# Kernel tuning notes

Measured on AMD Instinct MI355X. Metric: run time of the kernel, lower is better.

Reference implementation:

```python
import jax, jax.numpy as jnp
import numpy as np


def setup_inputs() -> dict:
    key = jax.random.key(0)
    kD, kx, kc = jax.random.split(key, 3)
    B, N, I, O = 8, 20000, 64, 64
    KM = 8 * 32  # k_bands * m_samples = 256
    D = jax.random.normal(kD, (B, N, KM), dtype=jnp.float32)
    x = jax.random.normal(kx, (B, N, I), dtype=jnp.float32)
    coefficients = jax.random.normal(kc, (1, O, I, KM), dtype=jnp.float32)
    return {"D": D, "x": x, "coefficients": coefficients}


def reference(D, x, coefficients):
    # D: (B, N, M), x: (B, N, I), coefficients: (1, O, I, M)
    # Original: C = diag_embed(coeff) -> (1,O,I,M,M); einsum('boimj,bomi->boij')
    # Since C is diagonal in (m, j), that einsum is an elementwise scale:
    #   C_Dt_x[b,o,i,m] = coeff[o,i,m] * Dt_x[b,m,i]
    # and the final contraction + channel-sum is:
    #   out[b,n,o] = (1/sqrt(M)) * sum_m D[b,n,m] * sum_i coeff[o,i,m] * Dt_x[b,m,i]
    M = D.shape[2]
    coeff = coefficients[0]                              # (O, I, M)
    Dt_x = jnp.einsum('bnm,bni->bmi', D, x)              # (B, M, I)
    S = jnp.einsum('oim,bmi->bom', coeff, Dt_x)          # (B, O, M)
    out = jnp.einsum('bnm,bom->bno', D, S) / jnp.sqrt(jnp.asarray(M, D.dtype))
    return out  # (B, N, O)
```

## Files before the change

kernel.cpp:

```cpp
#include <hip/hip_runtime.h>

#define B 8
#define N 20000
#define M 256
#define I 64
#define O 64
#define MI (M * I)
#define KT 32
#define PW (MI / 2)
#define SSS 264
#define MSW(m) ((m) ^ (((m) >> 3) & 7))

typedef __attribute__((ext_vector_type(8))) short   bf16x8;
typedef __attribute__((ext_vector_type(4))) float   f32x4;
typedef __attribute__((ext_vector_type(4))) unsigned int uint4v;

__device__ __forceinline__ unsigned pk2bf(float lo, float hi) {
    unsigned r;
    asm("v_cvt_pk_bf16_f32 %0, %1, %2" : "=v"(r) : "v"(lo), "v"(hi));
    return r;
}

__device__ __forceinline__ unsigned short f2bf(float v) {
    unsigned a = __float_as_uint(v);
    return (unsigned short)((a + 0x7fffu + ((a >> 16) & 1u)) >> 16);
}

__device__ __forceinline__ void gload16(const float* src, float* lds) {
    __builtin_amdgcn_global_load_lds(
        (const __attribute__((address_space(1))) void*)src,
        (__attribute__((address_space(3))) void*)lds, 16, 0, 0);
}

__global__ __launch_bounds__(256) void stage1(const float* __restrict__ Dg,
                                              const float* __restrict__ xg,
                                              unsigned* __restrict__ partial,
                                              int chunk) {
    const int b = blockIdx.y, s = blockIdx.x;
    const int n0 = s * chunk;
    const int nend = min(n0 + chunk, N);
    const int tid = threadIdx.x;
    const int lane = tid & 63;
    const int w = tid >> 6;
    const int lg = lane >> 4;
    const int l15 = lane & 15;

    __shared__ float sD[4][2][KT * 64];
    __shared__ unsigned short sX[4][4 * 64 * 8];

    f32x4 acc[4][4];
#pragma unroll
    for (int a = 0; a < 4; ++a)
#pragma unroll
        for (int v = 0; v < 4; ++v) acc[a][v] = (f32x4){0.f, 0.f, 0.f, 0.f};

    const float* Db = Dg + (size_t)b * N * M;
    const float* xb = xg + (size_t)b * N * I;

    const int steps = (nend > n0) ? (nend - n0) >> 5 : 0;

    auto issueD = [&](int t) {
        const int nb = n0 + t * KT;
        float* slot = &sD[w][t & 1][0];
        const float* src = Db + (size_t)(nb + lg) * M + (w << 6) + (l15 << 2);
#pragma unroll
        for (int j = 0; j < 8; ++j)
            gload16(src + (size_t)(4 * j) * M, slot + j * 256);
    };

    float4 xreg[8];
    auto loadX = [&](int t) {
        const float* xp = &xb[(size_t)(n0 + t * KT + 8 * lg) * I + 4 * l15];
#pragma unroll
        for (int q = 0; q < 8; ++q)
            xreg[q] = *(const float4*)(xp + (size_t)q * I);
    };

    unsigned short* wX = sX[w];

    if (steps > 0) {
        issueD(0);
        if (steps > 1) issueD(1);
        loadX(0);

        for (int t = 0; t < steps; ++t) {
            const int p = t & 1;
#pragma unroll
            for (int j = 0; j < 4; ++j) {
                uint4v cx;
#pragma unroll
                for (int e = 0; e < 4; ++e)
                    cx[e] = pk2bf(((const float*)&xreg[2 * e])[j],
                                  ((const float*)&xreg[2 * e + 1])[j]);
                *(uint4v*)&wX[((size_t)lg * 64 + MSW(4 * l15 + j)) * 8] = cx;
            }
            bf16x8 bfr[4];
#pragma unroll
            for (int v = 0; v < 4; ++v)
                bfr[v] = *(const bf16x8*)&wX[((size_t)lg * 64 + MSW(v * 16 + l15)) * 8];
            if (t + 1 < steps) loadX(t + 1);
            const float* slot = &sD[w][p][0];
#pragma unroll
            for (int sm = 0; sm < 4; ++sm) {
                float fr[8];
#pragma unroll
                for (int r = 0; r < 8; ++r)
                    fr[r] = slot[(8 * lg + r) * 64 + sm * 16 + l15];
                uint4v pk = {pk2bf(fr[0], fr[1]), pk2bf(fr[2], fr[3]),
                             pk2bf(fr[4], fr[5]), pk2bf(fr[6], fr[7])};
                bf16x8 afr = __builtin_bit_cast(bf16x8, pk);
#pragma unroll
                for (int v = 0; v < 4; ++v)
                    acc[sm][v] = __builtin_amdgcn_mfma_f32_16x16x32_bf16(
                        afr, bfr[v], acc[sm][v], 0, 0, 0);
            }
            if (t + 2 < steps) issueD(t + 2);
        }
    }

    unsigned* pp = partial + ((size_t)s * B + b) * PW + (size_t)w * 2048 + lane;
#pragma unroll
    for (int sm = 0; sm < 4; ++sm)
#pragma unroll
        for (int v = 0; v < 4; ++v)
#pragma unroll
            for (int rp = 0; rp < 2; ++rp)
                pp[(sm * 8 + v * 2 + rp) * 64] =
                    pk2bf(acc[sm][v][2 * rp], acc[sm][v][2 * rp + 1]);
}

__global__ __launch_bounds__(256) void reduce_partials(const unsigned* __restrict__ partial,
                                                       float* __restrict__ dtx,
                                                       int nsplit) {
    const int bb = blockIdx.y;
    const int j = blockIdx.x * 256 + threadIdx.x;
    const int w    = j >> 11;
    const int rem  = j & 2047;
    const int c    = rem >> 6;
    const int lane = rem & 63;
    const int sm = c >> 3, v = (c >> 1) & 3, rp = c & 1;
    const int lg = lane >> 4, l15 = lane & 15;
    const int m0 = w * 64 + sm * 16 + lg * 4 + 2 * rp;
    const int i  = v * 16 + l15;

    const unsigned* p = partial + (size_t)bb * PW + j;
    float s0 = 0.f, s1 = 0.f;
#pragma unroll 4
    for (int s = 0; s < nsplit; ++s) {
        const unsigned word = p[(size_t)s * B * PW];
        s0 += __uint_as_float(word << 16);
        s1 += __uint_as_float(word & 0xFFFF0000u);
    }
    dtx[(size_t)bb * MI + (size_t)m0 * I + i]       = s0;
    dtx[(size_t)bb * MI + (size_t)(m0 + 1) * I + i] = s1;
}

__global__ __launch_bounds__(256) void stage2(const float* __restrict__ coeff,
                                              const float* __restrict__ dtx,
                                              unsigned short* __restrict__ ST) {
    const int g = blockIdx.x * 256 + threadIdx.x;
    const int b = g >> 14;
    const int rem = g & 16383;
    const int o = rem >> 8;
    const int m = rem & 255;
    const float* dt = dtx + (size_t)b * MI + (size_t)m * I;
    const float* cf = coeff + (size_t)o * I * M + m;
    float acc = 0.f;
#pragma unroll 8
    for (int i = 0; i < I; ++i)
        acc = fmaf(cf[(size_t)i * M], dt[i], acc);
    ST[((size_t)b * O + o) * M + m] = f2bf(acc * 0.0625f);
}

__global__ __launch_bounds__(256) void stage3(const float* __restrict__ Dg,
                                              const unsigned short* __restrict__ STg,
                                              float* __restrict__ outg) {
    const int b = blockIdx.y;
    const int n0 = blockIdx.x * 256;
    const int tid = threadIdx.x;
    const int lane = tid & 63;
    const int w = tid >> 6;

    __shared__ unsigned short sS[64 * SSS];

    {
        const int o = tid >> 2, seg = (tid & 3) * 64;
        const unsigned short* src = STg + ((size_t)b * O + o) * M + seg;
        unsigned short* dst = &sS[o * SSS + seg];
#pragma unroll
        for (int c = 0; c < 8; ++c)
            *(uint4v*)&dst[c * 8] = *(const uint4v*)&src[c * 8];
    }

    f32x4 acc[4][4];
#pragma unroll
    for (int a = 0; a < 4; ++a)
#pragma unroll
        for (int v = 0; v < 4; ++v) acc[a][v] = (f32x4){0.f, 0.f, 0.f, 0.f};

    __syncthreads();

    const float* Db = Dg + (size_t)b * N * M;
    const int k8 = (lane >> 4) << 3;

#pragma unroll 1
    for (int ks = 0; ks < 8; ++ks) {
        const int kb = ks * 32 + k8;
        bf16x8 bfr[4];
#pragma unroll
        for (int v = 0; v < 4; ++v)
            bfr[v] = *(const bf16x8*)&sS[(v * 16 + (lane & 15)) * SSS + kb];
#pragma unroll
        for (int sn = 0; sn < 4; ++sn) {
            int n = n0 + w * 64 + sn * 16 + (lane & 15);
            n = min(n, N - 1);
            const float* ap = Db + (size_t)n * M + kb;
            const float4 f0 = *(const float4*)ap;
            const float4 f1 = *(const float4*)(ap + 4);
            uint4v pk = {pk2bf(f0.x, f0.y), pk2bf(f0.z, f0.w),
                         pk2bf(f1.x, f1.y), pk2bf(f1.z, f1.w)};
            bf16x8 afr = __builtin_bit_cast(bf16x8, pk);
#pragma unroll
            for (int v = 0; v < 4; ++v)
                acc[sn][v] = __builtin_amdgcn_mfma_f32_16x16x32_bf16(
                    afr, bfr[v], acc[sn][v], 0, 0, 0);
        }
    }

#pragma unroll
    for (int sn = 0; sn < 4; ++sn)
#pragma unroll
        for (int v = 0; v < 4; ++v)
#pragma unroll
            for (int r = 0; r < 4; ++r) {
                const int n = n0 + w * 64 + sn * 16 + ((lane >> 4) << 2) + r;
                if (n < N)
                    outg[((size_t)b * N + n) * O + v * 16 + (lane & 15)] = acc[sn][v][r];
            }
}

extern "C" void kernel_launch(void* const* d_in, const int* in_sizes, int n_in,
                              void* d_out, int out_size, void* d_ws, size_t ws_size,
                              hipStream_t stream) {
    const float* Dg    = (const float*)d_in[0];
    const float* xg    = (const float*)d_in[1];
    const float* coeff = (const float*)d_in[2];
    float* outg = (float*)d_out;

    float* base = (float*)d_ws;
    float* dtx = base;
    unsigned short* ST = (unsigned short*)(base + B * MI);
    unsigned* partial = (unsigned*)(base + B * MI + B * MI / 2);

    const size_t fixed = (size_t)B * MI * 4 + (size_t)B * MI * 2;
    const size_t per   = (size_t)B * PW * sizeof(unsigned);
    int cap = 1;
    if (ws_size > fixed) {
        size_t c = (ws_size - fixed) / per;
        cap = (int)(c < 1 ? 1 : (c > 64 ? 64 : c));
    }
    int chunk = (((N + cap - 1) / cap) + KT - 1) & ~(KT - 1);
    int split = (N + chunk - 1) / chunk;

    stage1<<<dim3(split, B), 256, 0, stream>>>(Dg, xg, partial, chunk);
    reduce_partials<<<dim3(PW / 256, B), 256, 0, stream>>>(partial, dtx, split);
    stage2<<<dim3((B * O * M) / 256), 256, 0, stream>>>(coeff, dtx, ST);
    stage3<<<dim3((N + 255) / 256, B), 256, 0, stream>>>(Dg, ST, outg);
}
```

Baseline: 91.50 us.

## Fuse partial reduction with coefficient contraction using shared-memory Dt_x tile

Merges the split-K partial reduction and the stage2 coefficient contraction into one kernel. Each block reduces a 32-row slice of Dt_x into shared memory and then computes all output channels for those rows. This removes a kernel launch and the global round trip of the fp32 Dt_x buffer. The trade-off is that the grid shrinks to 64 blocks, each doing far more serial partial loads, which can underuse the GPU's memory bandwidth.

New measurement: 131.0 us. 1.43x slower.

```diff
diff --git a/kernel.cpp b/kernel.cpp
--- a/kernel.cpp
+++ b/kernel.cpp
@@ -129,47 +129,55 @@
                     pk2bf(acc[sm][v][2 * rp], acc[sm][v][2 * rp + 1]);
 }
 
-__global__ __launch_bounds__(256) void reduce_partials(const unsigned* __restrict__ partial,
-                                                       float* __restrict__ dtx,
-                                                       int nsplit) {
+__global__ __launch_bounds__(256) void reduce_stage2(const unsigned* __restrict__ partial,
+                                                     const float* __restrict__ coeff,
+                                                     unsigned short* __restrict__ ST,
+                                                     int nsplit) {
+    const int mg = blockIdx.x;
     const int bb = blockIdx.y;
-    const int j = blockIdx.x * 256 + threadIdx.x;
-    const int w    = j >> 11;
-    const int rem  = j & 2047;
-    const int c    = rem >> 6;
-    const int lane = rem & 63;
-    const int sm = c >> 3, v = (c >> 1) & 3, rp = c & 1;
-    const int lg = lane >> 4, l15 = lane & 15;
-    const int m0 = w * 64 + sm * 16 + lg * 4 + 2 * rp;
-    const int i  = v * 16 + l15;
-
-    const unsigned* p = partial + (size_t)bb * PW + j;
-    float s0 = 0.f, s1 = 0.f;
+    const int tid = threadIdx.x;
+
+    __shared__ float dtx[32][65];
+
+    const int w = mg >> 1;
+#pragma unroll
+    for (int h = 0; h < 4; ++h) {
+        const int u = tid + h * 256;
+        const int smq  = u >> 9;
+        const int v    = (u >> 7) & 3;
+        const int rp   = (u >> 6) & 1;
+        const int lane = u & 63;
+        const int sm = (mg & 1) * 2 + smq;
+        const int j = w * 2048 + (sm * 8 + v * 2 + rp) * 64 + lane;
+        const unsigned* p = partial + (size_t)bb * PW + j;
+        float s0 = 0.f, s1 = 0.f;
 #pragma unroll 4
-    for (int s = 0; s < nsplit; ++s) {
-        const unsigned word = p[(size_t)s * B * PW];
-        s0 += __uint_as_float(word << 16);
-        s1 += __uint_as_float(word & 0xFFFF0000u);
-    }
-    dtx[(size_t)bb * MI + (size_t)m0 * I + i]       = s0;
-    dtx[(size_t)bb * MI + (size_t)(m0 + 1) * I + i] = s1;
-}
-
-__global__ __launch_bounds__(256) void stage2(const float* __restrict__ coeff,
-                                              const float* __restrict__ dtx,
-                                              unsigned short* __restrict__ ST) {
-    const int g = blockIdx.x * 256 + threadIdx.x;
-    const int b = g >> 14;
-    const int rem = g & 16383;
-    const int o = rem >> 8;
-    const int m = rem & 255;
-    const float* dt = dtx + (size_t)b * MI + (size_t)m * I;
-    const float* cf = coeff + (size_t)o * I * M + m;
-    float acc = 0.f;
+        for (int s = 0; s < nsplit; ++s) {
+            const unsigned word = p[(size_t)s * B * PW];
+            s0 += __uint_as_float(word << 16);
+            s1 += __uint_as_float(word & 0xFFFF0000u);
+        }
+        const int lg = lane >> 4, l15 = lane & 15;
+        const int mloc = smq * 16 + lg * 4 + 2 * rp;
+        const int i    = v * 16 + l15;
+        dtx[mloc][i]     = s0;
+        dtx[mloc + 1][i] = s1;
+    }
+    __syncthreads();
+
+    const int mloc  = tid & 31;
+    const int m     = mg * 32 + mloc;
+    const int obase = (tid >> 5) * 8;
+#pragma unroll
+    for (int oo = 0; oo < 8; ++oo) {
+        const int o = obase + oo;
+        const float* cf = coeff + (size_t)o * I * M + m;
+        float acc = 0.f;
 #pragma unroll 8
-    for (int i = 0; i < I; ++i)
-        acc = fmaf(cf[(size_t)i * M], dt[i], acc);
-    ST[((size_t)b * O + o) * M + m] = f2bf(acc * 0.0625f);
+        for (int i = 0; i < I; ++i)
+            acc = fmaf(cf[(size_t)i * M], dtx[mloc][i], acc);
+        ST[((size_t)bb * O + o) * M + m] = f2bf(acc * 0.0625f);
+    }
 }
 
 __global__ __launch_bounds__(256) void stage3(const float* __restrict__ Dg,
@@ -247,12 +255,10 @@
     const float* coeff = (const float*)d_in[2];
     float* outg = (float*)d_out;
 
-    float* base = (float*)d_ws;
-    float* dtx = base;
-    unsigned short* ST = (unsigned short*)(base + B * MI);
-    unsigned* partial = (unsigned*)(base + B * MI + B * MI / 2);
-
-    const size_t fixed = (size_t)B * MI * 4 + (size_t)B * MI * 2;
+    unsigned short* ST = (unsigned short*)d_ws;
+    unsigned* partial  = (unsigned*)((char*)d_ws + (size_t)B * O * M * 2);
+
+    const size_t fixed = (size_t)B * O * M * 2;
     const size_t per   = (size_t)B * PW * sizeof(unsigned);
     int cap = 1;
     if (ws_size > fixed) {
@@ -263,7 +269,6 @@
     int split = (N + chunk - 1) / chunk;
 
     stage1<<<dim3(split, B), 256, 0, stream>>>(Dg, xg, partial, chunk);
-    reduce_partials<<<dim3(PW / 256, B), 256, 0, stream>>>(partial, dtx, split);
-    stage2<<<dim3((B * O * M) / 256), 256, 0, stream>>>(coeff, dtx, ST);
+    reduce_stage2<<<dim3(M / 32, B), 256, 0, stream>>>(partial, coeff, ST, split);
     stage3<<<dim3((N + 255) / 256, B), 256, 0, stream>>>(Dg, ST, outg);
 }
```
